# Kernel optimization log

Hardware: AMD Instinct MI355X
Metric: run time of the kernel (lower is better)

Reference implementation:

```python
import jax, jax.numpy as jnp
import numpy as np


def _generate_fitpack_knots(x, k):
    # FITPACK-style knots: k+1 copies of x[0], k+1 copies of x[-1],
    # interior knots are length-k moving averages of x[1:-1].
    n = x.shape[0]
    n_interior = n - k - 1  # number of interior knots
    win_sum = x[1:1 + n_interior]
    for j in range(1, k):  # k is a small static int (e.g. 3)
        win_sum = win_sum + x[1 + j:1 + j + n_interior]
    interior = win_sum / k
    head = jnp.full((k + 1,), x[0], dtype=x.dtype)
    tail = jnp.full((k + 1,), x[-1], dtype=x.dtype)
    return jnp.concatenate([head, interior, tail])


def _safe_div(num, den):
    # torch.nan_to_num_(num/den): 0/0 -> 0, x/0 -> 0
    den_safe = jnp.where(den == 0, jnp.ones_like(den), den)
    return jnp.where(den == 0, jnp.zeros_like(num), num / den_safe)


def _bspline_basis_natural(x, k, t):
    n = x.shape[0]
    m = t.shape[0] - k - 1
    xc = x[:, None]  # [n, 1]
    # zeroth-order basis: indicator of knot interval, with boundary fixes
    b = ((t[None, :m] <= xc) & (xc < t[None, 1:m + 1])).astype(x.dtype)
    b = b.at[:, 0].set(jnp.where(x < t[1], jnp.ones_like(x), b[:, 0]))
    b = b.at[:, -1].set(jnp.where(x >= t[-2], jnp.ones_like(x), b[:, -1]))
    zeros_col = jnp.zeros((n, 1), dtype=x.dtype)
    # de Boor recursion over degree d = 1..k (k is static and small)
    for d in range(1, k + 1):
        L = _safe_div(xc - t[None, :m], (t[d:m + d] - t[:m])[None, :])
        R = _safe_div(t[None, d + 1:m + d + 1] - xc,
                      (t[d + 1:m + d + 1] - t[1:m + 1])[None, :])
        b_shift = jnp.concatenate([b[:, 1:], zeros_col], axis=1)
        b = L * b + R * b_shift
    return b  # [n, m]


def setup_inputs() -> dict:
    key = jax.random.key(0)
    N = 4096
    x = jnp.sort(jax.random.uniform(key, (N,), dtype=jnp.float32) * 10.0)
    s = jnp.asarray(1e-3, dtype=jnp.float32)
    return {"x": x, "s": s, "k": 3}


def reference(x, s, k):
    knots = _generate_fitpack_knots(x, k)
    basis_matrix = _bspline_basis_natural(x, k, knots)  # [n, m]
    m = basis_matrix.shape[-1]
    B_T_B = basis_matrix.T @ basis_matrix + s * jnp.eye(m, dtype=basis_matrix.dtype)
    return (knots, basis_matrix, B_T_B)
```

## Files before the change

### kernel.cpp

```cpp
#include <hip/hip_runtime.h>

#define K 3

__global__ void zero_fill(float* __restrict__ out, long long n4, long long n) {
    long long i = (long long)blockIdx.x * blockDim.x + threadIdx.x;
    long long stride = (long long)gridDim.x * blockDim.x;
    float4 z = make_float4(0.f, 0.f, 0.f, 0.f);
    float4* o4 = (float4*)out;
    for (long long j = i; j < n4; j += stride) o4[j] = z;
    long long tail = n4 * 4;
    for (long long j = tail + i; j < n; j += stride) out[j] = 0.f;
}

__global__ void knots_kernel(const float* __restrict__ x, float* __restrict__ t_out,
                             float* __restrict__ t_ws, int N) {
    int j = blockIdx.x * blockDim.x + threadIdx.x;
    int nk = N + K + 1;
    if (j >= nk) return;
    float v;
    if (j <= K) {
        v = x[0];
    } else if (j >= N) {
        v = x[N - 1];
    } else {
        int i = j - (K + 1);
        v = (x[i + 1] + x[i + 2] + x[i + 3]) / 3.0f;
    }
    t_out[j] = v;
    t_ws[j] = v;
}

__global__ void basis_kernel(const float* __restrict__ x, const float* __restrict__ t,
                             float* __restrict__ Bout, float* __restrict__ vals_ws,
                             int* __restrict__ j0_ws, int N) {
    int i = blockIdx.x * blockDim.x + threadIdx.x;
    if (i >= N) return;
    float xi = x[i];
    int nk = N + K + 1;

    int lo = 0, hi = nk;
    while (lo < hi) { int mid = (lo + hi) >> 1; if (t[mid] <= xi) lo = mid + 1; else hi = mid; }
    int j0 = lo - 1;
    if (j0 > N - 1) j0 = N - 1;
    if (j0 < K) j0 = K;
    int c0 = j0 - K;

    float b[K + 2];
    #pragma unroll
    for (int w = 0; w < K + 2; ++w) b[w] = 0.f;
    b[K] = 1.f;

    #pragma unroll
    for (int d = 1; d <= K; ++d) {
        float nb[K + 1];
        #pragma unroll
        for (int w = 0; w <= K; ++w) {
            int j = c0 + w;
            float tj   = t[j];
            float tjd  = t[j + d];
            float tj1  = t[j + 1];
            float tjd1 = t[j + d + 1];
            float denL = tjd - tj;
            float L = (denL == 0.f) ? 0.f : (xi - tj) / denL;
            float denR = tjd1 - tj1;
            float R = (denR == 0.f) ? 0.f : (tjd1 - xi) / denR;
            nb[w] = L * b[w] + R * b[w + 1];
        }
        #pragma unroll
        for (int w = 0; w <= K; ++w) b[w] = nb[w];
    }

    j0_ws[i] = j0;
    #pragma unroll
    for (int w = 0; w <= K; ++w) {
        vals_ws[i * (K + 1) + w] = b[w];
        Bout[(long long)i * N + (c0 + w)] = b[w];
    }
}

__global__ void btb_kernel(const float* __restrict__ vals, const int* __restrict__ j0arr,
                           const float* __restrict__ s_ptr, float* __restrict__ BTB, int N) {
    int ci = blockIdx.x * blockDim.x + threadIdx.x;
    if (ci >= N) return;

    int lo = 0, hi = N;
    while (lo < hi) { int mid = (lo + hi) >> 1; if (j0arr[mid] < ci) lo = mid + 1; else hi = mid; }
    int rlo = lo;
    hi = N;
    int target = ci + K + 1;
    while (lo < hi) { int mid = (lo + hi) >> 1; if (j0arr[mid] < target) lo = mid + 1; else hi = mid; }
    int rhi = lo;

    float acc[K + 1] = {0.f, 0.f, 0.f, 0.f};
    for (int r = rlo; r < rhi; ++r) {
        int c0r = j0arr[r] - K;
        int wi = ci - c0r;
        float v = vals[r * (K + 1) + wi];
        #pragma unroll
        for (int o = 0; o <= K; ++o) {
            int wj = wi + o;
            if (wj <= K) acc[o] += v * vals[r * (K + 1) + wj];
        }
    }

    float s = *s_ptr;
    long long base = (long long)ci * N;
    BTB[base + ci] = acc[0] + s;
    #pragma unroll
    for (int o = 1; o <= K; ++o) {
        if (ci + o < N) {
            BTB[base + ci + o] = acc[o];
            BTB[(long long)(ci + o) * N + ci] = acc[o];
        }
    }
}

extern "C" void kernel_launch(void* const* d_in, const int* in_sizes, int n_in,
                              void* d_out, int out_size, void* d_ws, size_t ws_size,
                              hipStream_t stream) {
    const float* x = (const float*)d_in[0];
    const float* s = (const float*)d_in[1];
    int N = in_sizes[0];
    int nk = N + K + 1;

    float* out = (float*)d_out;
    float* out_knots = out;
    float* out_B = out + nk;
    float* out_BTB = out_B + (long long)N * N;

    float* t_ws = (float*)d_ws;
    float* vals_ws = t_ws + nk;
    int* j0_ws = (int*)(vals_ws + (long long)N * (K + 1));

    long long total = (long long)out_size;
    long long n4 = total / 4;
    zero_fill<<<2048, 256, 0, stream>>>(out, n4, total);

    int tb = 256;
    knots_kernel<<<(nk + tb - 1) / tb, tb, 0, stream>>>(x, out_knots, t_ws, N);
    basis_kernel<<<(N + tb - 1) / tb, tb, 0, stream>>>(x, t_ws, out_B, vals_ws, j0_ws, N);
    btb_kernel<<<(N + tb - 1) / tb, tb, 0, stream>>>(vals_ws, j0_ws, s, out_BTB, N);
}
```

Baseline: 44.35 us.

## Fuse zero-fill with sparse writes and compute knots inline

Removes the separate zero-fill pass over the whole output. Instead, a per-row writer kernel emits each row of the B and BTB matrices once, with the nonzero band values placed inline, so the large dense outputs are written only one time. The separate knots kernel is also dropped: knots are computed on the fly from x inside the basis kernel. The BTB band is staged in a compact workspace first. The risks are extra recomputation during the binary search and the assumption that N is a multiple of 4 for the float4 row writes.

```diff
diff --git a/kernel.cpp b/kernel.cpp
--- a/kernel.cpp
+++ b/kernel.cpp
@@ -2,44 +2,24 @@
 
 #define K 3
 
-__global__ void zero_fill(float* __restrict__ out, long long n4, long long n) {
-    long long i = (long long)blockIdx.x * blockDim.x + threadIdx.x;
-    long long stride = (long long)gridDim.x * blockDim.x;
-    float4 z = make_float4(0.f, 0.f, 0.f, 0.f);
-    float4* o4 = (float4*)out;
-    for (long long j = i; j < n4; j += stride) o4[j] = z;
-    long long tail = n4 * 4;
-    for (long long j = tail + i; j < n; j += stride) out[j] = 0.f;
+__device__ __forceinline__ float tfun(const float* __restrict__ x, int j, int N) {
+    if (j <= K) return x[0];
+    if (j >= N) return x[N - 1];
+    return (x[j - 3] + x[j - 2] + x[j - 1]) / 3.0f;
 }
 
-__global__ void knots_kernel(const float* __restrict__ x, float* __restrict__ t_out,
-                             float* __restrict__ t_ws, int N) {
-    int j = blockIdx.x * blockDim.x + threadIdx.x;
-    int nk = N + K + 1;
-    if (j >= nk) return;
-    float v;
-    if (j <= K) {
-        v = x[0];
-    } else if (j >= N) {
-        v = x[N - 1];
-    } else {
-        int i = j - (K + 1);
-        v = (x[i + 1] + x[i + 2] + x[i + 3]) / 3.0f;
-    }
-    t_out[j] = v;
-    t_ws[j] = v;
-}
-
-__global__ void basis_kernel(const float* __restrict__ x, const float* __restrict__ t,
-                             float* __restrict__ Bout, float* __restrict__ vals_ws,
-                             int* __restrict__ j0_ws, int N) {
+__global__ void k1_basis(const float* __restrict__ x, float* __restrict__ out_knots,
+                         float* __restrict__ vals, int* __restrict__ j0arr, int N) {
     int i = blockIdx.x * blockDim.x + threadIdx.x;
     if (i >= N) return;
-    float xi = x[i];
     int nk = N + K + 1;
 
+    out_knots[i] = tfun(x, i, N);
+    if (i < nk - N) out_knots[N + i] = x[N - 1];
+
+    float xi = x[i];
     int lo = 0, hi = nk;
-    while (lo < hi) { int mid = (lo + hi) >> 1; if (t[mid] <= xi) lo = mid + 1; else hi = mid; }
+    while (lo < hi) { int mid = (lo + hi) >> 1; if (tfun(x, mid, N) <= xi) lo = mid + 1; else hi = mid; }
     int j0 = lo - 1;
     if (j0 > N - 1) j0 = N - 1;
     if (j0 < K) j0 = K;
@@ -56,10 +36,10 @@
         #pragma unroll
         for (int w = 0; w <= K; ++w) {
             int j = c0 + w;
-            float tj   = t[j];
-            float tjd  = t[j + d];
-            float tj1  = t[j + 1];
-            float tjd1 = t[j + d + 1];
+            float tj   = tfun(x, j, N);
+            float tjd  = tfun(x, j + d, N);
+            float tj1  = tfun(x, j + 1, N);
+            float tjd1 = tfun(x, j + d + 1, N);
             float denL = tjd - tj;
             float L = (denL == 0.f) ? 0.f : (xi - tj) / denL;
             float denR = tjd1 - tj1;
@@ -70,47 +50,97 @@
         for (int w = 0; w <= K; ++w) b[w] = nb[w];
     }
 
-    j0_ws[i] = j0;
-    #pragma unroll
-    for (int w = 0; w <= K; ++w) {
-        vals_ws[i * (K + 1) + w] = b[w];
-        Bout[(long long)i * N + (c0 + w)] = b[w];
-    }
+    j0arr[i] = j0;
+    *(float4*)(vals + i * 4) = make_float4(b[0], b[1], b[2], b[3]);
 }
 
-__global__ void btb_kernel(const float* __restrict__ vals, const int* __restrict__ j0arr,
-                           const float* __restrict__ s_ptr, float* __restrict__ BTB, int N) {
+__global__ void k2_band(const float* __restrict__ vals, const int* __restrict__ j0arr,
+                        const float* __restrict__ s_ptr, float* __restrict__ band, int N) {
     int ci = blockIdx.x * blockDim.x + threadIdx.x;
     if (ci >= N) return;
 
     int lo = 0, hi = N;
     while (lo < hi) { int mid = (lo + hi) >> 1; if (j0arr[mid] < ci) lo = mid + 1; else hi = mid; }
     int rlo = lo;
-    hi = N;
-    int target = ci + K + 1;
-    while (lo < hi) { int mid = (lo + hi) >> 1; if (j0arr[mid] < target) lo = mid + 1; else hi = mid; }
+    hi = N; int tgt = ci + K + 1;
+    while (lo < hi) { int mid = (lo + hi) >> 1; if (j0arr[mid] < tgt) lo = mid + 1; else hi = mid; }
     int rhi = lo;
 
-    float acc[K + 1] = {0.f, 0.f, 0.f, 0.f};
+    float acc[2 * K + 1];
+    #pragma unroll
+    for (int a = 0; a < 2 * K + 1; ++a) acc[a] = 0.f;
+
     for (int r = rlo; r < rhi; ++r) {
-        int c0r = j0arr[r] - K;
-        int wi = ci - c0r;
-        float v = vals[r * (K + 1) + wi];
+        int wi = ci - (j0arr[r] - K);
+        float4 v4 = *(const float4*)(vals + r * 4);
+        float v = (wi == 0) ? v4.x : (wi == 1) ? v4.y : (wi == 2) ? v4.z : v4.w;
         #pragma unroll
-        for (int o = 0; o <= K; ++o) {
+        for (int o = -K; o <= K; ++o) {
             int wj = wi + o;
-            if (wj <= K) acc[o] += v * vals[r * (K + 1) + wj];
+            float w = (wj == 0) ? v4.x : (wj == 1) ? v4.y : (wj == 2) ? v4.z
+                    : (wj == 3) ? v4.w : 0.f;
+            acc[o + K] += v * w;
         }
     }
+    acc[K] += *s_ptr;
 
-    float s = *s_ptr;
-    long long base = (long long)ci * N;
-    BTB[base + ci] = acc[0] + s;
-    #pragma unroll
-    for (int o = 1; o <= K; ++o) {
-        if (ci + o < N) {
-            BTB[base + ci + o] = acc[o];
-            BTB[(long long)(ci + o) * N + ci] = acc[o];
+    *(float4*)(band + ci * 8)     = make_float4(acc[0], acc[1], acc[2], acc[3]);
+    *(float4*)(band + ci * 8 + 4) = make_float4(acc[4], acc[5], acc[6], 0.f);
+}
+
+__global__ __launch_bounds__(256) void k3_write(const float* __restrict__ vals,
+                                                const int* __restrict__ j0arr,
+                                                const float* __restrict__ band,
+                                                float* __restrict__ outB,
+                                                float* __restrict__ outBTB, int N) {
+    int bid = blockIdx.x;
+    int tid = threadIdx.x;
+    int fpr = N >> 2;
+
+    if (bid < N) {
+        int i = bid;
+        int c0 = j0arr[i] - K;
+        float4 v4 = *(const float4*)(vals + i * 4);
+        float4* rowp = (float4*)(outB + (long long)i * N);
+        int fw0 = c0 >> 2, fw1 = (c0 + K) >> 2;
+        for (int f = tid; f < fpr; f += 256) {
+            float4 z = make_float4(0.f, 0.f, 0.f, 0.f);
+            if (f == fw0 || f == fw1) {
+                int e0 = f * 4;
+                float e[4];
+                #pragma unroll
+                for (int l = 0; l < 4; ++l) {
+                    int d = e0 + l - c0;
+                    e[l] = (d == 0) ? v4.x : (d == 1) ? v4.y : (d == 2) ? v4.z
+                         : (d == 3) ? v4.w : 0.f;
+                }
+                z = make_float4(e[0], e[1], e[2], e[3]);
+            }
+            rowp[f] = z;
+        }
+    } else {
+        int ci = bid - N;
+        float4 b0 = *(const float4*)(band + ci * 8);
+        float4 b1 = *(const float4*)(band + ci * 8 + 4);
+        float4* rowp = (float4*)(outBTB + (long long)ci * N);
+        int wlo = ci - K; if (wlo < 0) wlo = 0;
+        int whi = ci + K; if (whi > N - 1) whi = N - 1;
+        int fw0 = wlo >> 2, fw1 = whi >> 2;
+        for (int f = tid; f < fpr; f += 256) {
+            float4 z = make_float4(0.f, 0.f, 0.f, 0.f);
+            if (f >= fw0 && f <= fw1) {
+                int e0 = f * 4;
+                float e[4];
+                #pragma unroll
+                for (int l = 0; l < 4; ++l) {
+                    int d = e0 + l - ci;
+                    e[l] = (d == -3) ? b0.x : (d == -2) ? b0.y : (d == -1) ? b0.z
+                         : (d ==  0) ? b0.w : (d ==  1) ? b1.x : (d ==  2) ? b1.y
+                         : (d ==  3) ? b1.z : 0.f;
+                }
+                z = make_float4(e[0], e[1], e[2], e[3]);
+            }
+            rowp[f] = z;
         }
     }
 }
@@ -128,16 +158,12 @@
     float* out_B = out + nk;
     float* out_BTB = out_B + (long long)N * N;
 
-    float* t_ws = (float*)d_ws;
-    float* vals_ws = t_ws + nk;
-    int* j0_ws = (int*)(vals_ws + (long long)N * (K + 1));
-
-    long long total = (long long)out_size;
-    long long n4 = total / 4;
-    zero_fill<<<2048, 256, 0, stream>>>(out, n4, total);
+    float* band_ws = (float*)d_ws;
+    float* vals_ws = band_ws + (long long)N * 8;
+    int* j0_ws = (int*)(vals_ws + (long long)N * 4);
 
     int tb = 256;
-    knots_kernel<<<(nk + tb - 1) / tb, tb, 0, stream>>>(x, out_knots, t_ws, N);
-    basis_kernel<<<(N + tb - 1) / tb, tb, 0, stream>>>(x, t_ws, out_B, vals_ws, j0_ws, N);
-    btb_kernel<<<(N + tb - 1) / tb, tb, 0, stream>>>(vals_ws, j0_ws, s, out_BTB, N);
+    k1_basis<<<(N + tb - 1) / tb, tb, 0, stream>>>(x, out_knots, vals_ws, j0_ws, N);
+    k2_band<<<(N + tb - 1) / tb, tb, 0, stream>>>(vals_ws, j0_ws, s, band_ws, N);
+    k3_write<<<2 * N, tb, 0, stream>>>(vals_ws, j0_ws, band_ws, out_B, out_BTB, N);
 }
```

New measurement: 47.21 us. 6.4% more time.
